# Kernel tuning notes

Hardware: AMD Instinct MI355X
Metric: run time of the kernel (lower is better)

The kernel has to match this reference:

```python
import jax, jax.numpy as jnp
import numpy as np


def setup_inputs() -> dict:
    key = jax.random.key(0)
    ks = jax.random.split(key, 8)
    B, T, U = 4, 256, 128
    De, Dp, D, V = 512, 512, 640, 1024
    s = lambda k, sh, fan: jax.random.normal(k, sh, dtype=jnp.float32) / np.sqrt(fan)
    return {
        "enc": jax.random.normal(ks[0], (B, T, De), dtype=jnp.float32),
        "pred": jax.random.normal(ks[1], (B, U, Dp), dtype=jnp.float32),
        "W_enc": s(ks[2], (De, D), De),
        "b_enc": jnp.zeros((D,), jnp.float32),
        "W_pred": s(ks[3], (Dp, D), Dp),
        "b_pred": jnp.zeros((D,), jnp.float32),
        "W_joint": s(ks[4], (D, V), D),
        "b_joint": jnp.zeros((V,), jnp.float32),
    }


def reference(enc, pred, W_enc, b_enc, W_pred, b_pred, W_joint, b_joint):
    # f: [B,T,D], g: [B,U,D]
    f = jnp.einsum("bte,ed->btd", enc, W_enc) + b_enc
    g = jnp.einsum("bup,pd->bud", pred, W_pred) + b_pred
    # broadcast-add over the T x U lattice, tanh activation
    joint = jnp.tanh(f[:, :, None, :] + g[:, None, :, :])  # [B,T,U,D]
    # final projection to num_classes
    out = jnp.einsum("btud,dv->btuv", joint, W_joint) + b_joint  # [B,T,U,V]
    return out
```

## Files before the change

kernel.cpp:

```cpp
#include <hip/hip_runtime.h>
#include <hip/hip_bf16.h>
#include <stdint.h>

typedef unsigned short u16;
typedef __attribute__((ext_vector_type(8))) __bf16 bf16x8;
typedef __attribute__((ext_vector_type(4))) float f32x4;
typedef __attribute__((ext_vector_type(8))) unsigned short u16x8;
typedef __attribute__((ext_vector_type(4))) unsigned int u32x4;

static __device__ __forceinline__ u16 f2bf(float x) {
  __hip_bfloat16 h = __float2bfloat16(x);
  u16 u;
  __builtin_memcpy(&u, &h, 2);
  return u;
}

static __device__ __forceinline__ float fast_tanh(float x) {
  float e = __expf(2.0f * x);
  return 1.0f - 2.0f * __builtin_amdgcn_rcpf(e + 1.0f);
}

static __device__ __forceinline__ void gload_lds16(const void* g, void* l) {
  __builtin_amdgcn_global_load_lds(
      (const __attribute__((address_space(1))) unsigned int*)g,
      (__attribute__((address_space(3))) unsigned int*)l, 16, 0, 0);
}

static __device__ __forceinline__ int swz(int row, int byte_in_row) {
  return row * 128 + (byte_in_row ^ ((row & 7) << 4));
}

__global__ __launch_bounds__(256) void transpose_cast_kernel(
    const float* __restrict__ in, u16* __restrict__ out, int K, int N) {
  int n = blockIdx.x;
  for (int k = threadIdx.x; k < K; k += 256) {
    out[(size_t)n * K + k] = f2bf(in[(size_t)k * N + n]);
  }
}

__global__ __launch_bounds__(256) void linear_kernel(
    const float* __restrict__ A, const u16* __restrict__ Wt,
    const float* __restrict__ bias, float* __restrict__ out) {
  __shared__ u16 sA[64 * 64];
  __shared__ u16 sB[64 * 64];
  const int t = threadIdx.x;
  const int bx = blockIdx.x;
  const int m0 = (bx / 10) * 64;
  const int n0 = (bx % 10) * 64;
  const int lane = t & 63, wid = t >> 6;
  const int wr = wid >> 1, wc = wid & 1;
  const int l15 = lane & 15, lk8 = (lane >> 4) << 3;

  const int srow = t >> 2;
  const int kc = (t & 3) << 4;

  f32x4 acc[2][2] = {};

  for (int k0 = 0; k0 < 512; k0 += 64) {
    {
      const float4* gp = (const float4*)(A + (size_t)(m0 + srow) * 512 + k0 + kc);
      u16 tmp[16];
#pragma unroll
      for (int i = 0; i < 4; ++i) {
        float4 v = gp[i];
        tmp[i * 4 + 0] = f2bf(v.x);
        tmp[i * 4 + 1] = f2bf(v.y);
        tmp[i * 4 + 2] = f2bf(v.z);
        tmp[i * 4 + 3] = f2bf(v.w);
      }
      *(u16x8*)((char*)sA + swz(srow, kc * 2)) = *(u16x8*)&tmp[0];
      *(u16x8*)((char*)sA + swz(srow, kc * 2 + 16)) = *(u16x8*)&tmp[8];
    }
    {
      const int off = (t & 3) << 5;
      const char* gsrc = (const char*)Wt + ((size_t)(n0 + srow) * 512 + k0) * 2 + off;
      u32x4 q0 = *(const u32x4*)gsrc;
      u32x4 q1 = *(const u32x4*)(gsrc + 16);
      *(u32x4*)((char*)sB + swz(srow, off)) = q0;
      *(u32x4*)((char*)sB + swz(srow, off + 16)) = q1;
    }
    __syncthreads();
#pragma unroll
    for (int kh = 0; kh < 2; ++kh) {
      const int kbyte = kh * 64 + lk8 * 2;
      bf16x8 av[2], bv[2];
#pragma unroll
      for (int mf = 0; mf < 2; ++mf)
        av[mf] = *(const bf16x8*)((char*)sA + swz(wr * 32 + mf * 16 + l15, kbyte));
#pragma unroll
      for (int nf = 0; nf < 2; ++nf)
        bv[nf] = *(const bf16x8*)((char*)sB + swz(wc * 32 + nf * 16 + l15, kbyte));
#pragma unroll
      for (int mf = 0; mf < 2; ++mf)
#pragma unroll
        for (int nf = 0; nf < 2; ++nf)
          acc[mf][nf] = __builtin_amdgcn_mfma_f32_16x16x32_bf16(
              av[mf], bv[nf], acc[mf][nf], 0, 0, 0);
    }
    __syncthreads();
  }

  const int r4 = (lane >> 4) << 2;
#pragma unroll
  for (int nf = 0; nf < 2; ++nf) {
    const int nc = n0 + wc * 32 + nf * 16 + l15;
    const float bjv = bias[nc];
#pragma unroll
    for (int mf = 0; mf < 2; ++mf) {
      const int mr = m0 + wr * 32 + mf * 16 + r4;
#pragma unroll
      for (int r = 0; r < 4; ++r)
        out[(size_t)(mr + r) * 640 + nc] = acc[mf][nf][r] + bjv;
    }
  }
}

__global__ __launch_bounds__(256) void joint_kernel(
    const float* __restrict__ f, const float* __restrict__ g,
    u16* __restrict__ joint, int m_base) {
  int idx = blockIdx.x * 256 + threadIdx.x;
  int row = idx / 80;
  int kc = (idx % 80) * 8;
  int m = m_base + row;
  int bt = m >> 7;
  int b = bt >> 8;
  int u = m & 127;
  const float4* fp = (const float4*)(f + (size_t)bt * 640 + kc);
  const float4* gp = (const float4*)(g + ((size_t)(b * 128 + u)) * 640 + kc);
  u16 tmp[8];
#pragma unroll
  for (int i = 0; i < 2; ++i) {
    float4 fv = fp[i];
    float4 gv = gp[i];
    tmp[i * 4 + 0] = f2bf(fast_tanh(fv.x + gv.x));
    tmp[i * 4 + 1] = f2bf(fast_tanh(fv.y + gv.y));
    tmp[i * 4 + 2] = f2bf(fast_tanh(fv.z + gv.z));
    tmp[i * 4 + 3] = f2bf(fast_tanh(fv.w + gv.w));
  }
  *(u16x8*)(joint + (size_t)row * 640 + kc) = *(u16x8*)&tmp[0];
}

__global__ __launch_bounds__(512, 2) void gemm256_kernel(
    const u16* __restrict__ A,
    const u16* __restrict__ Bt,
    const float* __restrict__ bias,
    float* __restrict__ out,
    int m_base, int mtiles) {
  extern __shared__ char smem[];
  const int t = threadIdx.x;
  const int lane = t & 63, wid = t >> 6;

  const int nwg = mtiles * 4;
  const int bid = blockIdx.x;
  const int q = nwg >> 3, r = nwg & 7;
  const int xcd = bid & 7, local = bid >> 3;
  const int wgid = (xcd < r ? xcd * (q + 1) : r * (q + 1) + (xcd - r) * q) + local;
  const int mt = wgid >> 2, nt = wgid & 3;

  const int wr = wid >> 2, wc = wid & 3;
  const int l15 = lane & 15;
  const int xr = (lane & 7) << 4;
  const int cb_hi = (lane >> 4) << 4;

  const int srow = t >> 3;
  const int xc = ((t & 7) ^ ((t >> 3) & 7)) << 4;
  const u16* aSrc[4];
  const u16* bSrc[4];
#pragma unroll
  for (int j = 0; j < 4; ++j) {
    const int row = j * 64 + srow;
    aSrc[j] = A + (size_t)(mt * 256 + row) * 640 + (xc >> 1);
    bSrc[j] = Bt + (size_t)(nt * 256 + row) * 640 + (xc >> 1);
  }
  const int sdst = wid * 1024;

  f32x4 acc[8][4] = {};

#pragma unroll
  for (int j = 0; j < 4; ++j) {
    gload_lds16(aSrc[j], smem + j * 8192 + sdst);
    gload_lds16(bSrc[j], smem + 32768 + j * 8192 + sdst);
  }
  __syncthreads();

  for (int tt = 0; tt < 10; ++tt) {
    const int bufo = (tt & 1) * 65536;
    if (tt < 9) {
      const int ke = (tt + 1) * 64;
      const int nbufo = bufo ^ 65536;
#pragma unroll
      for (int j = 0; j < 4; ++j) {
        gload_lds16(aSrc[j] + ke, smem + nbufo + j * 8192 + sdst);
        gload_lds16(bSrc[j] + ke, smem + nbufo + 32768 + j * 8192 + sdst);
      }
    }
    const char* sA = smem + bufo;
    const char* sB = smem + bufo + 32768;
    bf16x8 bv[4][2];
#pragma unroll
    for (int nf = 0; nf < 4; ++nf)
#pragma unroll
      for (int kk = 0; kk < 2; ++kk) {
        const int row = wc * 64 + nf * 16 + l15;
        const int cb = kk * 64 + cb_hi;
        bv[nf][kk] = *(const bf16x8*)(sB + row * 128 + (cb ^ xr));
      }
#pragma unroll
    for (int qm = 0; qm < 2; ++qm) {
      bf16x8 av[4][2];
#pragma unroll
      for (int mi = 0; mi < 4; ++mi)
#pragma unroll
        for (int kk = 0; kk < 2; ++kk) {
          const int row = wr * 128 + (qm * 4 + mi) * 16 + l15;
          const int cb = kk * 64 + cb_hi;
          av[mi][kk] = *(const bf16x8*)(sA + row * 128 + (cb ^ xr));
        }
      __builtin_amdgcn_s_setprio(1);
#pragma unroll
      for (int mi = 0; mi < 4; ++mi)
#pragma unroll
        for (int nf = 0; nf < 4; ++nf)
#pragma unroll
          for (int kk = 0; kk < 2; ++kk)
            acc[qm * 4 + mi][nf] = __builtin_amdgcn_mfma_f32_16x16x32_bf16(
                av[mi][kk], bv[nf][kk], acc[qm * 4 + mi][nf], 0, 0, 0);
      __builtin_amdgcn_s_setprio(0);
    }
    if (tt < 9) __syncthreads();
  }

  const int r4 = (lane >> 4) << 2;
#pragma unroll
  for (int nf = 0; nf < 4; ++nf) {
    const int v = nt * 256 + wc * 64 + nf * 16 + l15;
    const float bjv = bias[v];
#pragma unroll
    for (int mf = 0; mf < 8; ++mf) {
      const size_t m = (size_t)m_base + (size_t)mt * 256 + wr * 128 + mf * 16 + r4;
#pragma unroll
      for (int rr = 0; rr < 4; ++rr)
        out[(m + rr) * 1024 + v] = acc[mf][nf][rr] + bjv;
    }
  }
}

__global__ __launch_bounds__(512) void fused_joint_kernel(
    const float* __restrict__ f, const float* __restrict__ g,
    const u16* __restrict__ Wjt, const float* __restrict__ bj,
    float* __restrict__ out) {
  __shared__ u16 sA[128 * 64];
  __shared__ u16 sB[256 * 64];
  const int t = threadIdx.x;
  const int bt = blockIdx.x;
  const int b = bt >> 8;
  const int v0 = blockIdx.y << 8;
  const float* frow = f + (size_t)bt * 640;
  const float* gbase = g + (size_t)b * 128 * 640;

  const int lane = t & 63, wid = t >> 6;
  const int wr = wid >> 2, wc = wid & 3;
  const int l15 = lane & 15, lk8 = (lane >> 4) << 3;

  const int au = t >> 2;
  const int akc = (t & 3) << 4;
  const int bn = t >> 1;
  const int boff = (t & 1) << 6;

  f32x4 acc[4][4] = {};

  for (int k0 = 0; k0 < 640; k0 += 64) {
    {
      const float4* gp = (const float4*)(gbase + (size_t)au * 640 + k0 + akc);
      const float4* fp = (const float4*)(frow + k0 + akc);
      u16 tmp[16];
#pragma unroll
      for (int i = 0; i < 4; ++i) {
        float4 gv = gp[i];
        float4 fv = fp[i];
        tmp[i * 4 + 0] = f2bf(fast_tanh(gv.x + fv.x));
        tmp[i * 4 + 1] = f2bf(fast_tanh(gv.y + fv.y));
        tmp[i * 4 + 2] = f2bf(fast_tanh(gv.z + fv.z));
        tmp[i * 4 + 3] = f2bf(fast_tanh(gv.w + fv.w));
      }
      *(u16x8*)((char*)sA + swz(au, akc * 2)) = *(u16x8*)&tmp[0];
      *(u16x8*)((char*)sA + swz(au, akc * 2 + 16)) = *(u16x8*)&tmp[8];
    }
    {
      const char* gsrc = (const char*)Wjt + ((size_t)(v0 + bn) * 640 + k0) * 2 + boff;
#pragma unroll
      for (int i = 0; i < 4; ++i) {
        u32x4 qv = *(const u32x4*)(gsrc + i * 16);
        *(u32x4*)((char*)sB + swz(bn, boff + i * 16)) = qv;
      }
    }
    __syncthreads();
#pragma unroll
    for (int kh = 0; kh < 2; ++kh) {
      const int kbyte = kh * 64 + lk8 * 2;
      bf16x8 av[4], bv[4];
#pragma unroll
      for (int mf = 0; mf < 4; ++mf)
        av[mf] = *(const bf16x8*)((char*)sA + swz(wr * 64 + mf * 16 + l15, kbyte));
#pragma unroll
      for (int nf = 0; nf < 4; ++nf)
        bv[nf] = *(const bf16x8*)((char*)sB + swz(wc * 64 + nf * 16 + l15, kbyte));
#pragma unroll
      for (int mf = 0; mf < 4; ++mf)
#pragma unroll
        for (int nf = 0; nf < 4; ++nf)
          acc[mf][nf] = __builtin_amdgcn_mfma_f32_16x16x32_bf16(
              av[mf], bv[nf], acc[mf][nf], 0, 0, 0);
    }
    __syncthreads();
  }

  const int r4 = (lane >> 4) << 2;
#pragma unroll
  for (int nf = 0; nf < 4; ++nf) {
    const int v = v0 + wc * 64 + nf * 16 + l15;
    const float bjv = bj[v];
#pragma unroll
    for (int mf = 0; mf < 4; ++mf) {
      const int u = wr * 64 + mf * 16 + r4;
      const size_t o = ((size_t)bt * 128 + u) * 1024 + v;
#pragma unroll
      for (int rr = 0; rr < 4; ++rr)
        out[o + (size_t)rr * 1024] = acc[mf][nf][rr] + bjv;
    }
  }
}

extern "C" void kernel_launch(void* const* d_in, const int* in_sizes, int n_in,
                              void* d_out, int out_size, void* d_ws, size_t ws_size,
                              hipStream_t stream) {
  const float* enc = (const float*)d_in[0];
  const float* pred = (const float*)d_in[1];
  const float* W_enc = (const float*)d_in[2];
  const float* b_enc = (const float*)d_in[3];
  const float* W_pred = (const float*)d_in[4];
  const float* b_pred = (const float*)d_in[5];
  const float* W_joint = (const float*)d_in[6];
  const float* b_joint = (const float*)d_in[7];
  float* out = (float*)d_out;

  char* ws = (char*)d_ws;
  float* f = (float*)ws;
  float* gbuf = (float*)(ws + 2621440);
  u16* Wet = (u16*)(ws + 2621440 + 1310720);
  u16* Wpt = (u16*)(ws + 2621440 + 1310720 + 655360);
  u16* Wjt = (u16*)(ws + 2621440 + 1310720 + 2 * 655360);
  const size_t fixed = 2621440 + 1310720 + 2 * 655360 + 1310720;
  u16* joint = (u16*)(ws + fixed);

  transpose_cast_kernel<<<640, 256, 0, stream>>>(W_enc, Wet, 512, 640);
  transpose_cast_kernel<<<640, 256, 0, stream>>>(W_pred, Wpt, 512, 640);
  transpose_cast_kernel<<<1024, 256, 0, stream>>>(W_joint, Wjt, 640, 1024);

  linear_kernel<<<16 * 10, 256, 0, stream>>>(enc, Wet, b_enc, f);
  linear_kernel<<<8 * 10, 256, 0, stream>>>(pred, Wpt, b_pred, gbuf);

  const long TOTAL_M = 131072;
  long maxrows = ws_size > fixed ? (long)((ws_size - fixed) / 1280) : 0;
  maxrows &= ~255L;

  if (maxrows >= 16384) {
    (void)hipFuncSetAttribute((const void*)gemm256_kernel,
                              hipFuncAttributeMaxDynamicSharedMemorySize, 131072);
    long CH = maxrows >= TOTAL_M ? TOTAL_M : maxrows;
    for (long m0 = 0; m0 < TOTAL_M; m0 += CH) {
      long R = TOTAL_M - m0 < CH ? TOTAL_M - m0 : CH;
      int mtiles = (int)(R / 256);
      joint_kernel<<<(int)(R / 128) * 40, 256, 0, stream>>>(f, gbuf, joint, (int)m0);
      gemm256_kernel<<<mtiles * 4, 512, 131072, stream>>>(joint, Wjt, b_joint, out,
                                                          (int)m0, mtiles);
    }
  } else {
    fused_joint_kernel<<<dim3(1024, 4), 512, 0, stream>>>(f, gbuf, Wjt, b_joint, out);
  }
}
```

Before: 345.7 us.

## Use 4-stage K=32 LDS ring with vmcnt-based waits in joint GEMM

```diff
diff --git a/kernel.cpp b/kernel.cpp
--- a/kernel.cpp
+++ b/kernel.cpp
@@ -159,76 +159,58 @@
 
   const int wr = wid >> 2, wc = wid & 3;
   const int l15 = lane & 15;
-  const int xr = (lane & 7) << 4;
-  const int cb_hi = (lane >> 4) << 4;
-
-  const int srow = t >> 3;
-  const int xc = ((t & 7) ^ ((t >> 3) & 7)) << 4;
-  const u16* aSrc[4];
-  const u16* bSrc[4];
-#pragma unroll
-  for (int j = 0; j < 4; ++j) {
-    const int row = j * 64 + srow;
-    aSrc[j] = A + (size_t)(mt * 256 + row) * 640 + (xc >> 1);
-    bSrc[j] = Bt + (size_t)(nt * 256 + row) * 640 + (xc >> 1);
-  }
-  const int sdst = wid * 1024;
+  const int colbyte = (((lane >> 4) ^ ((l15 >> 1) & 3)) << 4);
+
+  const int srow = lane >> 2;
+  const int scol = ((lane & 3) ^ ((lane >> 3) & 3)) << 3;
+  const u16* aS = A + (size_t)(mt * 256 + wid * 16 + srow) * 640 + scol;
+  const u16* bS = Bt + (size_t)(nt * 256 + wid * 16 + srow) * 640 + scol;
+  const int ldsbase = wid * 1024;
+
+#define STAGE(kt, slot)                                              \
+  do {                                                               \
+    const int ko_ = (kt) * 32;                                       \
+    char* sb_ = smem + (slot) * 32768;                               \
+    gload_lds16(aS + ko_, sb_ + ldsbase);                            \
+    gload_lds16(aS + 128 * 640 + ko_, sb_ + 8192 + ldsbase);         \
+    gload_lds16(bS + ko_, sb_ + 16384 + ldsbase);                    \
+    gload_lds16(bS + 128 * 640 + ko_, sb_ + 24576 + ldsbase);        \
+  } while (0)
 
   f32x4 acc[8][4] = {};
 
-#pragma unroll
-  for (int j = 0; j < 4; ++j) {
-    gload_lds16(aSrc[j], smem + j * 8192 + sdst);
-    gload_lds16(bSrc[j], smem + 32768 + j * 8192 + sdst);
-  }
-  __syncthreads();
-
-  for (int tt = 0; tt < 10; ++tt) {
-    const int bufo = (tt & 1) * 65536;
-    if (tt < 9) {
-      const int ke = (tt + 1) * 64;
-      const int nbufo = bufo ^ 65536;
-#pragma unroll
-      for (int j = 0; j < 4; ++j) {
-        gload_lds16(aSrc[j] + ke, smem + nbufo + j * 8192 + sdst);
-        gload_lds16(bSrc[j] + ke, smem + nbufo + 32768 + j * 8192 + sdst);
-      }
-    }
-    const char* sA = smem + bufo;
-    const char* sB = smem + bufo + 32768;
-    bf16x8 bv[4][2];
+  STAGE(0, 0);
+  STAGE(1, 1);
+  STAGE(2, 2);
+
+  for (int tt = 0; tt < 20; ++tt) {
+    asm volatile("s_waitcnt vmcnt(8)" ::: "memory");
+    __builtin_amdgcn_s_barrier();
+    __builtin_amdgcn_sched_barrier(0);
+    const int kt = (tt + 3 > 19) ? 19 : tt + 3;
+    STAGE(kt, (tt + 3) & 3);
+
+    const char* sA = smem + (tt & 3) * 32768;
+    const char* sB = sA + 16384;
+    bf16x8 av[8], bv[4];
 #pragma unroll
     for (int nf = 0; nf < 4; ++nf)
-#pragma unroll
-      for (int kk = 0; kk < 2; ++kk) {
-        const int row = wc * 64 + nf * 16 + l15;
-        const int cb = kk * 64 + cb_hi;
-        bv[nf][kk] = *(const bf16x8*)(sB + row * 128 + (cb ^ xr));
-      }
-#pragma unroll
-    for (int qm = 0; qm < 2; ++qm) {
-      bf16x8 av[4][2];
-#pragma unroll
-      for (int mi = 0; mi < 4; ++mi)
-#pragma unroll
-        for (int kk = 0; kk < 2; ++kk) {
-          const int row = wr * 128 + (qm * 4 + mi) * 16 + l15;
-          const int cb = kk * 64 + cb_hi;
-          av[mi][kk] = *(const bf16x8*)(sA + row * 128 + (cb ^ xr));
-        }
-      __builtin_amdgcn_s_setprio(1);
-#pragma unroll
-      for (int mi = 0; mi < 4; ++mi)
-#pragma unroll
-        for (int nf = 0; nf < 4; ++nf)
-#pragma unroll
-          for (int kk = 0; kk < 2; ++kk)
-            acc[qm * 4 + mi][nf] = __builtin_amdgcn_mfma_f32_16x16x32_bf16(
-                av[mi][kk], bv[nf][kk], acc[qm * 4 + mi][nf], 0, 0, 0);
-      __builtin_amdgcn_s_setprio(0);
-    }
-    if (tt < 9) __syncthreads();
-  }
+      bv[nf] = *(const bf16x8*)(sB + (wc * 64 + nf * 16 + l15) * 64 + colbyte);
+#pragma unroll
+    for (int mi = 0; mi < 8; ++mi)
+      av[mi] = *(const bf16x8*)(sA + (wr * 128 + mi * 16 + l15) * 64 + colbyte);
+
+    __builtin_amdgcn_s_setprio(1);
+#pragma unroll
+    for (int mi = 0; mi < 8; ++mi)
+#pragma unroll
+      for (int nf = 0; nf < 4; ++nf)
+        acc[mi][nf] = __builtin_amdgcn_mfma_f32_16x16x32_bf16(
+            av[mi], bv[nf], acc[mi][nf], 0, 0, 0);
+    __builtin_amdgcn_s_setprio(0);
+    __builtin_amdgcn_sched_barrier(0);
+  }
+#undef STAGE
 
   const int r4 = (lane >> 4) << 2;
 #pragma unroll
```

Result: slower. 367.5 us (+6.3%).
